# Performance work log

Measured on AMD Instinct MI355X. Metric: run time of the kernel, lower is better.

The kernel has to match this reference:

```python
import jax, jax.numpy as jnp
import numpy as np

D_MODEL = 160
D_STATE = 64
D_CONV = 12
N_BLOCKS = 8
CONV_K = 9
D_INNER = 2 * D_MODEL          # expand=2 -> 320
DT_RANK = (D_MODEL + 15) // 16  # ceil(160/16) = 10
B, T = 16, 2048


def setup_inputs() -> dict:
    key = jax.random.key(0)
    ks = jax.random.split(key, 10)
    rn = lambda k, shape, s=0.02: jax.random.normal(k, shape, dtype=jnp.float32) * s
    x = jax.random.normal(ks[0], (B, T, 1), dtype=jnp.float32)
    pre_w = rn(ks[1], (D_MODEL, 1, CONV_K), 0.3)
    pre_b = jnp.zeros((D_MODEL,), jnp.float32)
    ln_g = jnp.ones((N_BLOCKS, D_MODEL), jnp.float32)
    ln_b = jnp.zeros((N_BLOCKS, D_MODEL), jnp.float32)
    in_w = rn(ks[2], (N_BLOCKS, 2 * D_INNER, D_MODEL))
    conv_w = rn(ks[3], (N_BLOCKS, D_INNER, D_CONV), 0.1)
    conv_b = jnp.zeros((N_BLOCKS, D_INNER), jnp.float32)
    xproj_w = rn(ks[4], (N_BLOCKS, DT_RANK + 2 * D_STATE, D_INNER))
    dt_w = rn(ks[5], (N_BLOCKS, D_INNER, DT_RANK), 0.1)
    # softplus-inverse of dt_init=0.01 (mamba-style init) so softplus(dt_b) ~ 0.01
    dt_b = jnp.full((N_BLOCKS, D_INNER), float(np.log(np.expm1(0.01))), jnp.float32)
    A_log = jnp.log(jnp.tile(jnp.arange(1, D_STATE + 1, dtype=jnp.float32)[None, None, :],
                             (N_BLOCKS, D_INNER, 1)))
    D_skip = jnp.ones((N_BLOCKS, D_INNER), jnp.float32)
    out_w = rn(ks[6], (N_BLOCKS, D_MODEL, D_INNER))
    head_w = rn(ks[7], (1, D_MODEL))
    head_b = jnp.zeros((1,), jnp.float32)
    return dict(x=x, pre_w=pre_w, pre_b=pre_b, ln_g=ln_g, ln_b=ln_b, in_w=in_w,
                conv_w=conv_w, conv_b=conv_b, xproj_w=xproj_w, dt_w=dt_w, dt_b=dt_b,
                A_log=A_log, D_skip=D_skip, out_w=out_w, head_w=head_w, head_b=head_b)


def _layernorm(x, g, b, eps=1e-5):
    m = jnp.mean(x, -1, keepdims=True)
    v = jnp.var(x, -1, keepdims=True)
    return (x - m) * jax.lax.rsqrt(v + eps) * g + b


def _mamba(x, in_w, conv_w, conv_b, xproj_w, dt_w, dt_b, A_log, D_skip, out_w):
    # x: (B, L, d_model)
    bsz, L, _ = x.shape
    xz = jnp.einsum('bld,ed->ble', x, in_w)          # (B, L, 2*D_INNER)
    u, z = jnp.split(xz, 2, axis=-1)
    # depthwise causal conv over time
    u_c = jnp.moveaxis(u, 1, 2)                       # (B, D_INNER, L)
    u_c = jax.lax.conv_general_dilated(
        u_c, conv_w[:, None, :], (1,), [(D_CONV - 1, 0)],
        dimension_numbers=('NCH', 'OIH', 'NCH'), feature_group_count=D_INNER)
    u = jax.nn.silu(jnp.moveaxis(u_c, 1, 2) + conv_b)  # (B, L, D_INNER)
    x_dbl = jnp.einsum('bld,ed->ble', u, xproj_w)      # (B, L, DT_RANK + 2*D_STATE)
    dt, Bm, Cm = jnp.split(x_dbl, [DT_RANK, DT_RANK + D_STATE], axis=-1)
    delta = jax.nn.softplus(jnp.einsum('blr,dr->bld', dt, dt_w) + dt_b)  # (B, L, D_INNER)
    A = -jnp.exp(A_log)                                # (D_INNER, D_STATE)

    def step(h, ins):
        d_t, B_t, C_t, u_t = ins                       # (B,di),(B,ds),(B,ds),(B,di)
        dA = jnp.exp(d_t[:, :, None] * A)              # (B, di, ds)
        h = h * dA + (d_t * u_t)[:, :, None] * B_t[:, None, :]
        y = jnp.einsum('bds,bs->bd', h, C_t)
        return h, y

    tm = lambda a: jnp.moveaxis(a, 1, 0)               # time-major
    h0 = jnp.zeros((bsz, D_INNER, D_STATE), x.dtype)
    _, ys = jax.lax.scan(step, h0, (tm(delta), tm(Bm), tm(Cm), tm(u)))
    y = jnp.moveaxis(ys, 0, 1) + u * D_skip            # (B, L, D_INNER)
    y = y * jax.nn.silu(z)
    return jnp.einsum('bld,ed->ble', y, out_w)         # (B, L, d_model)


def reference(x, pre_w, pre_b, ln_g, ln_b, in_w, conv_w, conv_b, xproj_w,
              dt_w, dt_b, A_log, D_skip, out_w, head_w, head_b):
    # conv stem: (B,T,1) -> (B,1,T) -> conv -> (B,d_model,T)
    h = jax.lax.conv_general_dilated(
        jnp.moveaxis(x, 1, 2), pre_w, (1,), [(CONV_K // 2, CONV_K // 2)],
        dimension_numbers=('NCH', 'OIH', 'NCH')) + pre_b[None, :, None]
    h = jax.nn.gelu(jnp.moveaxis(h, 1, 2), approximate=False)  # torch GELU exact
    for i in range(N_BLOCKS):
        res = h
        y = _layernorm(h, ln_g[i], ln_b[i])
        y = _mamba(y, in_w[i], conv_w[i], conv_b[i], xproj_w[i], dt_w[i],
                   dt_b[i], A_log[i], D_skip[i], out_w[i])
        h = y + res  # dropout is identity at inference
    out = jnp.einsum('bld,od->blo', h, head_w) + head_b
    return out[..., 0]                                 # (B, T)
```

## Files before the change

### kernel.cpp

```cpp
#include <hip/hip_runtime.h>
#include <math.h>

#define BATCH 16
#define TLEN 2048
#define NTOK (BATCH*TLEN)
#define DMODEL 160
#define DINNER 320
#define DSTATE 64
#define DTRANK 10
#define XDBL 138
#define DCONV 12
#define PREK 9
#define NBLK 8

typedef __attribute__((ext_vector_type(8))) short short8;
typedef __attribute__((ext_vector_type(4))) float floatx4;

__device__ __forceinline__ float sigmoidf_(float x) { return 1.f / (1.f + __expf(-x)); }
__device__ __forceinline__ unsigned short f2bf(float f) {
  union { float f; unsigned u; } v; v.f = f;
  unsigned r = v.u + 0x7FFF + ((v.u >> 16) & 1);
  return (unsigned short)(r >> 16);
}
__device__ __forceinline__ float bf2f(unsigned short s) {
  union { unsigned u; float f; } v; v.u = ((unsigned)s) << 16;
  return v.f;
}

__global__ __launch_bounds__(256)
void k_preconv(const float* __restrict__ x, const float* __restrict__ w,
               const float* __restrict__ bias, float* __restrict__ h) {
  int gid = blockIdx.x * 256 + threadIdx.x;
  if (gid >= NTOK * DMODEL) return;
  int c = gid % DMODEL;
  int tok = gid / DMODEL;
  int b = tok / TLEN, t = tok % TLEN;
  const float* xb = x + (size_t)b * TLEN;
  float acc = bias[c];
#pragma unroll
  for (int k = 0; k < PREK; ++k) {
    int tp = t + k - PREK / 2;
    float xv = (tp >= 0 && tp < TLEN) ? xb[tp] : 0.f;
    acc = fmaf(w[c * PREK + k], xv, acc);
  }
  h[gid] = 0.5f * acc * (1.f + erff(acc * 0.70710678118654752440f));
}

__global__ __launch_bounds__(256)
void k_cast(const float* __restrict__ iw, const float* __restrict__ xw,
            const float* __restrict__ ow, unsigned short* __restrict__ wbf) {
  int i = blockIdx.x * 256 + threadIdx.x;
  if (i < 102400) wbf[i] = f2bf(iw[i]);
  else if (i < 146560) wbf[i] = f2bf(xw[i - 102400]);
  else if (i < 197760) wbf[i] = f2bf(ow[i - 146560]);
}

__global__ __launch_bounds__(256)
void k_ln(const float* __restrict__ h, const float* __restrict__ g,
          const float* __restrict__ bb, unsigned short* __restrict__ y) {
  int row = blockIdx.x * 4 + (threadIdx.x >> 6);
  int lane = threadIdx.x & 63;
  const float* hr = h + (size_t)row * DMODEL;
  float v0 = hr[lane], v1 = hr[lane + 64];
  float v2 = (lane < DMODEL - 128) ? hr[lane + 128] : 0.f;
  float s = v0 + v1 + v2;
  float sq = v0 * v0 + v1 * v1 + v2 * v2;
#pragma unroll
  for (int off = 32; off; off >>= 1) {
    s += __shfl_xor(s, off);
    sq += __shfl_xor(sq, off);
  }
  float mean = s * (1.f / DMODEL);
  float var = sq * (1.f / DMODEL) - mean * mean;
  float rstd = rsqrtf(var + 1e-5f);
  unsigned short* yr = y + (size_t)row * DMODEL;
  yr[lane] = f2bf((v0 - mean) * rstd * g[lane] + bb[lane]);
  yr[lane + 64] = f2bf((v1 - mean) * rstd * g[lane + 64] + bb[lane + 64]);
  if (lane < DMODEL - 128)
    yr[lane + 128] = f2bf((v2 - mean) * rstd * g[lane + 128] + bb[lane + 128]);
}

__global__ __launch_bounds__(256)
void k_mm_in(const unsigned short* __restrict__ A, const unsigned short* __restrict__ Wb,
             float* __restrict__ xout, unsigned short* __restrict__ zout) {
  __shared__ short As[128 * 40];
  __shared__ short Ws[128 * 40];
  int tid = threadIdx.x;
  int m0 = blockIdx.y * 128, n0 = blockIdx.x * 128;
  int w = tid >> 6, lane = tid & 63;
  int rm = (w >> 1) * 64, cn = (w & 1) * 64;
  int lm = lane & 15, quad = lane >> 4;
  int r = tid >> 1, seg = tid & 1;
  const unsigned short* pA = A + (size_t)(m0 + r) * DMODEL + seg * 16;
  const unsigned short* pW = Wb + (size_t)(n0 + r) * DMODEL + seg * 16;
  floatx4 acc[4][4];
#pragma unroll
  for (int i = 0; i < 4; ++i)
#pragma unroll
    for (int j = 0; j < 4; ++j)
      acc[i][j] = (floatx4){0.f, 0.f, 0.f, 0.f};
  for (int kt = 0; kt < 5; ++kt) {
    uint4 a0 = *(const uint4*)(pA + kt * 32);
    uint4 a1 = *(const uint4*)(pA + kt * 32 + 8);
    uint4 w0 = *(const uint4*)(pW + kt * 32);
    uint4 w1 = *(const uint4*)(pW + kt * 32 + 8);
    *(short8*)&As[r * 40 + seg * 16]     = *(short8*)&a0;
    *(short8*)&As[r * 40 + seg * 16 + 8] = *(short8*)&a1;
    *(short8*)&Ws[r * 40 + seg * 16]     = *(short8*)&w0;
    *(short8*)&Ws[r * 40 + seg * 16 + 8] = *(short8*)&w1;
    __syncthreads();
    short8 af[4], wf[4];
#pragma unroll
    for (int i = 0; i < 4; ++i)
      af[i] = *(short8*)&As[(rm + i * 16 + lm) * 40 + quad * 8];
#pragma unroll
    for (int j = 0; j < 4; ++j)
      wf[j] = *(short8*)&Ws[(cn + j * 16 + lm) * 40 + quad * 8];
#pragma unroll
    for (int i = 0; i < 4; ++i)
#pragma unroll
      for (int j = 0; j < 4; ++j)
        acc[i][j] = __builtin_amdgcn_mfma_f32_16x16x32_bf16(af[i], wf[j], acc[i][j], 0, 0, 0);
    __syncthreads();
  }
#pragma unroll
  for (int i = 0; i < 4; ++i)
#pragma unroll
    for (int reg = 0; reg < 4; ++reg) {
      int m = m0 + rm + i * 16 + quad * 4 + reg;
#pragma unroll
      for (int j = 0; j < 4; ++j) {
        int n = n0 + cn + j * 16 + lm;
        float v = acc[i][j][reg];
        if (n < DINNER) xout[(size_t)m * DINNER + n] = v;
        else zout[(size_t)m * DINNER + n - DINNER] = f2bf(v);
      }
    }
}

__global__ __launch_bounds__(256)
void k_mm_g(const unsigned short* __restrict__ A, const unsigned short* __restrict__ Wb,
            float* __restrict__ C, const float* __restrict__ resid, int N, int K) {
  __shared__ short As[128 * 40];
  __shared__ short Ws[64 * 40];
  int tid = threadIdx.x;
  int m0 = blockIdx.y * 128, n0 = blockIdx.x * 64;
  int w = tid >> 6, lane = tid & 63;
  int rm = w * 32;
  int lm = lane & 15, quad = lane >> 4;
  int r = tid >> 1, seg = tid & 1;
  int wr = tid >> 2, wseg = tid & 3;
  bool wvld = (n0 + wr) < N;
  const unsigned short* pA = A + (size_t)(m0 + r) * K + seg * 16;
  const unsigned short* pW = Wb + (size_t)(wvld ? (n0 + wr) : 0) * K + wseg * 8;
  floatx4 acc[2][4];
#pragma unroll
  for (int i = 0; i < 2; ++i)
#pragma unroll
    for (int j = 0; j < 4; ++j)
      acc[i][j] = (floatx4){0.f, 0.f, 0.f, 0.f};
  int nk = K >> 5;
  for (int kt = 0; kt < nk; ++kt) {
    uint4 a0 = *(const uint4*)(pA + kt * 32);
    uint4 a1 = *(const uint4*)(pA + kt * 32 + 8);
    uint4 wv = wvld ? *(const uint4*)(pW + kt * 32)
                    : make_uint4(0u, 0u, 0u, 0u);
    *(short8*)&As[r * 40 + seg * 16]     = *(short8*)&a0;
    *(short8*)&As[r * 40 + seg * 16 + 8] = *(short8*)&a1;
    *(short8*)&Ws[wr * 40 + wseg * 8]    = *(short8*)&wv;
    __syncthreads();
    short8 af[2], wf[4];
#pragma unroll
    for (int i = 0; i < 2; ++i)
      af[i] = *(short8*)&As[(rm + i * 16 + lm) * 40 + quad * 8];
#pragma unroll
    for (int j = 0; j < 4; ++j)
      wf[j] = *(short8*)&Ws[(j * 16 + lm) * 40 + quad * 8];
#pragma unroll
    for (int i = 0; i < 2; ++i)
#pragma unroll
      for (int j = 0; j < 4; ++j)
        acc[i][j] = __builtin_amdgcn_mfma_f32_16x16x32_bf16(af[i], wf[j], acc[i][j], 0, 0, 0);
    __syncthreads();
  }
#pragma unroll
  for (int i = 0; i < 2; ++i)
#pragma unroll
    for (int reg = 0; reg < 4; ++reg) {
      int m = m0 + rm + i * 16 + quad * 4 + reg;
#pragma unroll
      for (int j = 0; j < 4; ++j) {
        int n = n0 + j * 16 + lm;
        if (n < N) {
          float v = acc[i][j][reg];
          if (resid) v += resid[(size_t)m * N + n];
          C[(size_t)m * N + n] = v;
        }
      }
    }
}

__global__ __launch_bounds__(256)
void k_mm_x(const unsigned short* __restrict__ A, const unsigned short* __restrict__ Wb,
            unsigned short* __restrict__ C) {
  const int N = XDBL, K = DINNER;
  __shared__ short As[128 * 40];
  __shared__ short Ws[64 * 40];
  int tid = threadIdx.x;
  int m0 = blockIdx.y * 128, n0 = blockIdx.x * 64;
  int w = tid >> 6, lane = tid & 63;
  int rm = w * 32;
  int lm = lane & 15, quad = lane >> 4;
  int r = tid >> 1, seg = tid & 1;
  int wr = tid >> 2, wseg = tid & 3;
  bool wvld = (n0 + wr) < N;
  const unsigned short* pA = A + (size_t)(m0 + r) * K + seg * 16;
  const unsigned short* pW = Wb + (size_t)(wvld ? (n0 + wr) : 0) * K + wseg * 8;
  floatx4 acc[2][4];
#pragma unroll
  for (int i = 0; i < 2; ++i)
#pragma unroll
    for (int j = 0; j < 4; ++j)
      acc[i][j] = (floatx4){0.f, 0.f, 0.f, 0.f};
  int nk = K >> 5;
  for (int kt = 0; kt < nk; ++kt) {
    uint4 a0 = *(const uint4*)(pA + kt * 32);
    uint4 a1 = *(const uint4*)(pA + kt * 32 + 8);
    uint4 wv = wvld ? *(const uint4*)(pW + kt * 32)
                    : make_uint4(0u, 0u, 0u, 0u);
    *(short8*)&As[r * 40 + seg * 16]     = *(short8*)&a0;
    *(short8*)&As[r * 40 + seg * 16 + 8] = *(short8*)&a1;
    *(short8*)&Ws[wr * 40 + wseg * 8]    = *(short8*)&wv;
    __syncthreads();
    short8 af[2], wf[4];
#pragma unroll
    for (int i = 0; i < 2; ++i)
      af[i] = *(short8*)&As[(rm + i * 16 + lm) * 40 + quad * 8];
#pragma unroll
    for (int j = 0; j < 4; ++j)
      wf[j] = *(short8*)&Ws[(j * 16 + lm) * 40 + quad * 8];
#pragma unroll
    for (int i = 0; i < 2; ++i)
#pragma unroll
      for (int j = 0; j < 4; ++j)
        acc[i][j] = __builtin_amdgcn_mfma_f32_16x16x32_bf16(af[i], wf[j], acc[i][j], 0, 0, 0);
    __syncthreads();
  }
#pragma unroll
  for (int i = 0; i < 2; ++i)
#pragma unroll
    for (int reg = 0; reg < 4; ++reg) {
      int m = m0 + rm + i * 16 + quad * 4 + reg;
#pragma unroll
      for (int j = 0; j < 4; ++j) {
        int n = n0 + j * 16 + lm;
        if (n < N) C[(size_t)m * N + n] = f2bf(acc[i][j][reg]);
      }
    }
}

__global__ __launch_bounds__(256)
void k_convT(const float* __restrict__ xbuf, const float* __restrict__ cw,
             const float* __restrict__ cb, unsigned short* __restrict__ uTb,
             unsigned short* __restrict__ ubf) {
  int t0 = blockIdx.x * 64, d0 = blockIdx.y * 64, b = blockIdx.z;
  __shared__ float xs[76 * 65];
  __shared__ float us[64 * 65];
  int tid = threadIdx.x, j = tid & 63, w = tid >> 6;
#pragma unroll
  for (int it = 0; it < 19; ++it) {
    int r = it * 4 + w;
    int t = t0 - (DCONV - 1) + r;
    xs[r * 65 + j] = (t >= 0 && t < TLEN)
        ? xbuf[((size_t)b * TLEN + t) * DINNER + d0 + j] : 0.f;
  }
  __syncthreads();
  float cwr[DCONV];
#pragma unroll
  for (int k = 0; k < DCONV; ++k) cwr[k] = cw[(d0 + j) * DCONV + k];
  float cbv = cb[d0 + j];
#pragma unroll
  for (int it = 0; it < 16; ++it) {
    int tl = it * 4 + w;
    float acc = cbv;
#pragma unroll
    for (int k = 0; k < DCONV; ++k)
      acc = fmaf(cwr[k], xs[(tl + k) * 65 + j], acc);
    us[tl * 65 + j] = acc * sigmoidf_(acc);
  }
  __syncthreads();
#pragma unroll
  for (int it = 0; it < 16; ++it) {
    int tr = it * 4 + w;
    ubf[((size_t)b * TLEN + t0 + tr) * DINNER + d0 + j] = f2bf(us[tr * 65 + j]);
  }
#pragma unroll
  for (int it = 0; it < 16; ++it) {
    int dl = it * 4 + w;
    uTb[((size_t)b * DINNER + d0 + dl) * TLEN + t0 + j] = f2bf(us[j * 65 + dl]);
  }
}

__global__ __launch_bounds__(256)
void k_pack(const unsigned short* __restrict__ zbuf, const unsigned short* __restrict__ xdbl,
            const float* __restrict__ dtw, const float* __restrict__ dtb,
            float* __restrict__ delT, unsigned short* __restrict__ szT) {
  int t0 = blockIdx.x * 64, d0 = blockIdx.y * 64, b = blockIdx.z;
  __shared__ float zs[64 * 65];
  __shared__ float xd[64 * 13];
  int tid = threadIdx.x, j = tid & 63, w = tid >> 6;
#pragma unroll
  for (int it = 0; it < 16; ++it) {
    int i = it * 4 + w;
    zs[i * 65 + j] = bf2f(zbuf[((size_t)b * TLEN + t0 + i) * DINNER + d0 + j]);
  }
  {
    int r = tid >> 2, c = tid & 3;
    size_t rowb = ((size_t)b * TLEN + t0 + r) * XDBL;
    for (int cc = c; cc < DTRANK; cc += 4)
      xd[r * 13 + cc] = bf2f(xdbl[rowb + cc]);
  }
  __syncthreads();
#pragma unroll
  for (int it = 0; it < 16; ++it) {
    int dl = it * 4 + w, d = d0 + dl;
    float acc = dtb[d];
    const float* wr = dtw + d * DTRANK;
#pragma unroll
    for (int rr = 0; rr < DTRANK; ++rr)
      acc = fmaf(xd[j * 13 + rr], wr[rr], acc);
    float del = (acc > 20.f) ? acc : log1pf(__expf(acc));
    size_t o = ((size_t)b * DINNER + d) * TLEN + t0 + j;
    delT[o] = del;
    float zv = zs[j * 65 + dl];
    szT[o] = f2bf(zv * sigmoidf_(zv));
  }
}

__global__ __launch_bounds__(256)
void k_scan(const float* __restrict__ delT, const unsigned short* __restrict__ uTb,
            const unsigned short* __restrict__ szT, const unsigned short* __restrict__ xdbl,
            const float* __restrict__ Alog, const float* __restrict__ Dskip,
            unsigned short* __restrict__ yTb) {
  int wave = threadIdx.x >> 6, lane = threadIdx.x & 63;
  int b = blockIdx.x / (DINNER / 4);
  int d = (blockIdx.x % (DINNER / 4)) * 4 + wave;
  __shared__ float ps_all[4][16 * 68];
  float* ps = ps_all[wave];
  float Al2 = -__expf(Alog[d * DSTATE + lane]) * 1.44269504088896340736f;
  float Dd = Dskip[d];
  size_t chan = ((size_t)b * DINNER + d) * TLEN;
  const float* pd = delT + chan;
  const unsigned short* pu = uTb + chan;
  const unsigned short* psz = szT + chan;
  unsigned short* py = yTb + chan;
  const unsigned short* xb = xdbl + (size_t)b * TLEN * XDBL + DTRANK + lane;
  float h = 0.f;
  int tl = lane & 15, qq = lane >> 4;
  for (int t0 = 0; t0 < TLEN; t0 += 16) {
#pragma unroll
    for (int t = 0; t < 16; ++t) {
      float del = pd[t0 + t];
      float uu = bf2f(pu[t0 + t]);
      const unsigned short* xr = xb + (size_t)(t0 + t) * XDBL;
      float Bv = bf2f(xr[0]), Cv = bf2f(xr[DSTATE]);
      h = fmaf(h, exp2f(del * Al2), del * uu * Bv);
      ps[t * 68 + lane] = h * Cv;
    }
    float p = 0.f;
    const floatx4* pr = (const floatx4*)&ps[tl * 68 + qq * 16];
#pragma unroll
    for (int i = 0; i < 4; ++i) {
      floatx4 v = pr[i];
      p += v[0] + v[1] + v[2] + v[3];
    }
    p += __shfl_xor(p, 16);
    p += __shfl_xor(p, 32);
    if (lane < 16) {
      int t = t0 + tl;
      float uu = bf2f(pu[t]);
      py[t] = f2bf((p + uu * Dd) * bf2f(psz[t]));
    }
  }
}

__global__ __launch_bounds__(256)
void k_t2b(const unsigned short* __restrict__ yTb, unsigned short* __restrict__ ybf) {
  int t0 = blockIdx.x * 64, d0 = blockIdx.y * 64, b = blockIdx.z;
  __shared__ unsigned short ls[64 * 66];
  int tid = threadIdx.x, j = tid & 63, w = tid >> 6;
#pragma unroll
  for (int it = 0; it < 16; ++it) {
    int dl = it * 4 + w;
    ls[dl * 66 + j] = yTb[((size_t)b * DINNER + d0 + dl) * TLEN + t0 + j];
  }
  __syncthreads();
#pragma unroll
  for (int it = 0; it < 16; ++it) {
    int tr = it * 4 + w;
    ybf[((size_t)b * TLEN + t0 + tr) * DINNER + d0 + j] = ls[j * 66 + tr];
  }
}

__global__ __launch_bounds__(256)
void k_head(const float* __restrict__ h, const float* __restrict__ hw,
            const float* __restrict__ hb, float* __restrict__ out) {
  int tok = blockIdx.x * 4 + (threadIdx.x >> 6);
  int lane = threadIdx.x & 63;
  const float* hr = h + (size_t)tok * DMODEL;
  float s = hr[lane] * hw[lane] + hr[lane + 64] * hw[lane + 64];
  if (lane < DMODEL - 128) s += hr[lane + 128] * hw[lane + 128];
#pragma unroll
  for (int off = 32; off; off >>= 1) s += __shfl_xor(s, off);
  if (lane == 0) out[tok] = s + hb[0];
}

extern "C" void kernel_launch(void* const* d_in, const int* in_sizes, int n_in,
                              void* d_out, int out_size, void* d_ws, size_t ws_size,
                              hipStream_t stream) {
  const float* x      = (const float*)d_in[0];
  const float* pre_w  = (const float*)d_in[1];
  const float* pre_b  = (const float*)d_in[2];
  const float* ln_g   = (const float*)d_in[3];
  const float* ln_b   = (const float*)d_in[4];
  const float* in_w   = (const float*)d_in[5];
  const float* conv_w = (const float*)d_in[6];
  const float* conv_b = (const float*)d_in[7];
  const float* xproj_w= (const float*)d_in[8];
  const float* dt_w   = (const float*)d_in[9];
  const float* dt_b   = (const float*)d_in[10];
  const float* A_log  = (const float*)d_in[11];
  const float* D_skip = (const float*)d_in[12];
  const float* out_w  = (const float*)d_in[13];
  const float* head_w = (const float*)d_in[14];
  const float* head_b = (const float*)d_in[15];
  float* out = (float*)d_out;

  float* ws = (float*)d_ws;
  float* h    = ws;
  unsigned short* xdbl_bf = (unsigned short*)(h + (size_t)NTOK * DMODEL);
  float* delT = (float*)(xdbl_bf + (size_t)NTOK * XDBL);
  unsigned short* uT_bf = (unsigned short*)(delT + (size_t)NTOK * DINNER);
  float* X    = (float*)(uT_bf + (size_t)NTOK * DINNER);
  float* Y    = X + (size_t)NTOK * DINNER;
  float* Z    = Y + (size_t)NTOK * DINNER / 2;
  unsigned short* wbf = (unsigned short*)(Z + (size_t)NTOK * DINNER / 2);

  float*          xbuf    = X;
  unsigned short* szT     = (unsigned short*)X;
  unsigned short* y_bf    = (unsigned short*)X;
  unsigned short* zbuf_bf = (unsigned short*)Y;
  unsigned short* yT_bf   = (unsigned short*)Y;
  unsigned short* lnxd_bf = (unsigned short*)Z;
  unsigned short* u_bf    = (unsigned short*)Z;
  unsigned short* w_in    = wbf;
  unsigned short* w_xp    = wbf + 102400;
  unsigned short* w_ou    = wbf + 146560;

  k_preconv<<<NTOK * DMODEL / 256, 256, 0, stream>>>(x, pre_w, pre_b, h);

  for (int L = 0; L < NBLK; ++L) {
    k_cast<<<773, 256, 0, stream>>>(
        in_w + (size_t)L * 640 * DMODEL, xproj_w + (size_t)L * XDBL * DINNER,
        out_w + (size_t)L * DMODEL * DINNER, wbf);
    k_ln<<<NTOK / 4, 256, 0, stream>>>(h, ln_g + L * DMODEL, ln_b + L * DMODEL, lnxd_bf);
    k_mm_in<<<dim3(5, NTOK / 128), 256, 0, stream>>>(lnxd_bf, w_in, xbuf, zbuf_bf);
    k_convT<<<dim3(TLEN / 64, DINNER / 64, BATCH), 256, 0, stream>>>(
        xbuf, conv_w + (size_t)L * DINNER * DCONV, conv_b + (size_t)L * DINNER,
        uT_bf, u_bf);
    k_mm_x<<<dim3(3, NTOK / 128), 256, 0, stream>>>(u_bf, w_xp, xdbl_bf);
    k_pack<<<dim3(TLEN / 64, DINNER / 64, BATCH), 256, 0, stream>>>(
        zbuf_bf, xdbl_bf, dt_w + (size_t)L * DINNER * DTRANK, dt_b + (size_t)L * DINNER,
        delT, szT);
    k_scan<<<BATCH * (DINNER / 4), 256, 0, stream>>>(
        delT, uT_bf, szT, xdbl_bf, A_log + (size_t)L * DINNER * DSTATE,
        D_skip + (size_t)L * DINNER, yT_bf);
    k_t2b<<<dim3(TLEN / 64, DINNER / 64, BATCH), 256, 0, stream>>>(yT_bf, y_bf);
    k_mm_g<<<dim3(3, NTOK / 128), 256, 0, stream>>>(y_bf, w_ou, h, h, DMODEL, DINNER);
  }

  k_head<<<NTOK / 4, 256, 0, stream>>>(h, head_w, head_b, out);
}
```

Measured before the change: 3.841 ms.

## Pack scan inputs: interleave B/C, precompute delta*u and gated skip term

The x-projection GEMM now writes its output with a padded row stride where each B and C value sits next to the other, so the scan loads both with one 32-bit read per lane per timestep. k_pack now precomputes (delta, delta*u) as a float2 and a packed bf16 pair (u*D*silu(z), silu(z)), so the scan's inner loop does fewer loads and the output becomes a single fma. This removes the scan's separate u, szT and Dskip reads. It costs a wider qT buffer, an extra uT read in k_pack, and workspace aliasing that was rearranged to match.

Measured after the change: 3.640 ms. 5.2% less time.

```diff
diff --git a/kernel.cpp b/kernel.cpp
--- a/kernel.cpp
+++ b/kernel.cpp
@@ -9,6 +9,7 @@
 #define DSTATE 64
 #define DTRANK 10
 #define XDBL 138
+#define XP 140
 #define DCONV 12
 #define PREK 9
 #define NBLK 8
@@ -25,6 +26,12 @@
 __device__ __forceinline__ float bf2f(unsigned short s) {
   union { unsigned u; float f; } v; v.u = ((unsigned)s) << 16;
   return v.f;
+}
+__device__ __forceinline__ float bflo(unsigned u) {
+  union { unsigned u; float f; } v; v.u = u << 16; return v.f;
+}
+__device__ __forceinline__ float bfhi(unsigned u) {
+  union { unsigned u; float f; } v; v.u = u & 0xFFFF0000u; return v.f;
 }
 
 __global__ __launch_bounds__(256)
@@ -254,7 +261,12 @@
 #pragma unroll
       for (int j = 0; j < 4; ++j) {
         int n = n0 + j * 16 + lm;
-        if (n < N) C[(size_t)m * N + n] = f2bf(acc[i][j][reg]);
+        if (n < N) {
+          int slot = (n < DTRANK) ? n
+                   : (n < DTRANK + DSTATE) ? 12 + 2 * (n - DTRANK)
+                                           : 13 + 2 * (n - DTRANK - DSTATE);
+          C[(size_t)m * XP + slot] = f2bf(acc[i][j][reg]);
+        }
       }
     }
 }
@@ -303,8 +315,10 @@
 
 __global__ __launch_bounds__(256)
 void k_pack(const unsigned short* __restrict__ zbuf, const unsigned short* __restrict__ xdbl,
+            const unsigned short* __restrict__ uTb,
             const float* __restrict__ dtw, const float* __restrict__ dtb,
-            float* __restrict__ delT, unsigned short* __restrict__ szT) {
+            const float* __restrict__ Dskip,
+            float2* __restrict__ qT, unsigned* __restrict__ eT) {
   int t0 = blockIdx.x * 64, d0 = blockIdx.y * 64, b = blockIdx.z;
   __shared__ float zs[64 * 65];
   __shared__ float xd[64 * 13];
@@ -316,7 +330,7 @@
   }
   {
     int r = tid >> 2, c = tid & 3;
-    size_t rowb = ((size_t)b * TLEN + t0 + r) * XDBL;
+    size_t rowb = ((size_t)b * TLEN + t0 + r) * XP;
     for (int cc = c; cc < DTRANK; cc += 4)
       xd[r * 13 + cc] = bf2f(xdbl[rowb + cc]);
   }
@@ -331,16 +345,19 @@
       acc = fmaf(xd[j * 13 + rr], wr[rr], acc);
     float del = (acc > 20.f) ? acc : log1pf(__expf(acc));
     size_t o = ((size_t)b * DINNER + d) * TLEN + t0 + j;
-    delT[o] = del;
+    float uv = bf2f(uTb[o]);
     float zv = zs[j * 65 + dl];
-    szT[o] = f2bf(zv * sigmoidf_(zv));
-  }
-}
-
-__global__ __launch_bounds__(256)
-void k_scan(const float* __restrict__ delT, const unsigned short* __restrict__ uTb,
-            const unsigned short* __restrict__ szT, const unsigned short* __restrict__ xdbl,
-            const float* __restrict__ Alog, const float* __restrict__ Dskip,
+    float ssz = zv * sigmoidf_(zv);
+    qT[o] = make_float2(del, del * uv);
+    unsigned lo = f2bf(uv * Dskip[d] * ssz);
+    unsigned hi = f2bf(ssz);
+    eT[o] = lo | (hi << 16);
+  }
+}
+
+__global__ __launch_bounds__(256)
+void k_scan(const float2* __restrict__ qT, const unsigned* __restrict__ eT,
+            const unsigned short* __restrict__ xdbl, const float* __restrict__ Alog,
             unsigned short* __restrict__ yTb) {
   int wave = threadIdx.x >> 6, lane = threadIdx.x & 63;
   int b = blockIdx.x / (DINNER / 4);
@@ -348,23 +365,20 @@
   __shared__ float ps_all[4][16 * 68];
   float* ps = ps_all[wave];
   float Al2 = -__expf(Alog[d * DSTATE + lane]) * 1.44269504088896340736f;
-  float Dd = Dskip[d];
   size_t chan = ((size_t)b * DINNER + d) * TLEN;
-  const float* pd = delT + chan;
-  const unsigned short* pu = uTb + chan;
-  const unsigned short* psz = szT + chan;
+  const float2* pq = qT + chan;
+  const unsigned* pe = eT + chan;
   unsigned short* py = yTb + chan;
-  const unsigned short* xb = xdbl + (size_t)b * TLEN * XDBL + DTRANK + lane;
+  const unsigned* xb = (const unsigned*)(xdbl + (size_t)b * TLEN * XP) + 6 + lane;
   float h = 0.f;
   int tl = lane & 15, qq = lane >> 4;
   for (int t0 = 0; t0 < TLEN; t0 += 16) {
 #pragma unroll
     for (int t = 0; t < 16; ++t) {
-      float del = pd[t0 + t];
-      float uu = bf2f(pu[t0 + t]);
-      const unsigned short* xr = xb + (size_t)(t0 + t) * XDBL;
-      float Bv = bf2f(xr[0]), Cv = bf2f(xr[DSTATE]);
-      h = fmaf(h, exp2f(del * Al2), del * uu * Bv);
+      float2 q = pq[t0 + t];
+      unsigned bc = xb[(size_t)(t0 + t) * (XP / 2)];
+      float Bv = bflo(bc), Cv = bfhi(bc);
+      h = fmaf(h, exp2f(q.x * Al2), q.y * Bv);
       ps[t * 68 + lane] = h * Cv;
     }
     float p = 0.f;
@@ -378,8 +392,8 @@
     p += __shfl_xor(p, 32);
     if (lane < 16) {
       int t = t0 + tl;
-      float uu = bf2f(pu[t]);
-      py[t] = f2bf((p + uu * Dd) * bf2f(psz[t]));
+      unsigned e = pe[t];
+      py[t] = f2bf(fmaf(p, bfhi(e), bflo(e)));
     }
   }
 }
@@ -439,20 +453,19 @@
   float* ws = (float*)d_ws;
   float* h    = ws;
   unsigned short* xdbl_bf = (unsigned short*)(h + (size_t)NTOK * DMODEL);
-  float* delT = (float*)(xdbl_bf + (size_t)NTOK * XDBL);
-  unsigned short* uT_bf = (unsigned short*)(delT + (size_t)NTOK * DINNER);
+  float2* qT  = (float2*)(xdbl_bf + (size_t)NTOK * XP);
+  unsigned short* uT_bf = (unsigned short*)(qT + (size_t)NTOK * DINNER);
   float* X    = (float*)(uT_bf + (size_t)NTOK * DINNER);
   float* Y    = X + (size_t)NTOK * DINNER;
-  float* Z    = Y + (size_t)NTOK * DINNER / 2;
-  unsigned short* wbf = (unsigned short*)(Z + (size_t)NTOK * DINNER / 2);
-
+  unsigned short* wbf = (unsigned short*)(Y + (size_t)NTOK * DINNER / 2);
+
+  unsigned short* lnxd_bf = (unsigned short*)qT;
+  unsigned short* u_bf    = (unsigned short*)qT;
   float*          xbuf    = X;
-  unsigned short* szT     = (unsigned short*)X;
+  unsigned*       eT      = (unsigned*)X;
   unsigned short* y_bf    = (unsigned short*)X;
   unsigned short* zbuf_bf = (unsigned short*)Y;
   unsigned short* yT_bf   = (unsigned short*)Y;
-  unsigned short* lnxd_bf = (unsigned short*)Z;
-  unsigned short* u_bf    = (unsigned short*)Z;
   unsigned short* w_in    = wbf;
   unsigned short* w_xp    = wbf + 102400;
   unsigned short* w_ou    = wbf + 146560;
@@ -470,11 +483,10 @@
         uT_bf, u_bf);
     k_mm_x<<<dim3(3, NTOK / 128), 256, 0, stream>>>(u_bf, w_xp, xdbl_bf);
     k_pack<<<dim3(TLEN / 64, DINNER / 64, BATCH), 256, 0, stream>>>(
-        zbuf_bf, xdbl_bf, dt_w + (size_t)L * DINNER * DTRANK, dt_b + (size_t)L * DINNER,
-        delT, szT);
+        zbuf_bf, xdbl_bf, uT_bf, dt_w + (size_t)L * DINNER * DTRANK,
+        dt_b + (size_t)L * DINNER, D_skip + (size_t)L * DINNER, qT, eT);
     k_scan<<<BATCH * (DINNER / 4), 256, 0, stream>>>(
-        delT, uT_bf, szT, xdbl_bf, A_log + (size_t)L * DINNER * DSTATE,
-        D_skip + (size_t)L * DINNER, yT_bf);
+        qT, eT, xdbl_bf, A_log + (size_t)L * DINNER * DSTATE, yT_bf);
     k_t2b<<<dim3(TLEN / 64, DINNER / 64, BATCH), 256, 0, stream>>>(yT_bf, y_bf);
     k_mm_g<<<dim3(3, NTOK / 128), 256, 0, stream>>>(y_bf, w_ou, h, h, DMODEL, DINNER);
   }
```
